# Optimization experiments

Measured on AMD Instinct MI355X. Metric: run time of the kernel, lower is better.

Reference implementation:

```python
import jax, jax.numpy as jnp
import numpy as np

N_NODES = 50000
N_EDGES = 800000
IN_DIM = 256
OUT_DIM = 128
NUM_CLASSES = 3


def setup_inputs() -> dict:
    key = jax.random.key(0)
    ks = jax.random.split(key, 8)
    x = jax.random.normal(ks[0], (N_NODES, IN_DIM), dtype=jnp.float32)
    edge_index = jax.random.randint(ks[1], (2, N_EDGES), 0, N_NODES, dtype=jnp.int64)
    # Linear W (no bias): torch stores [out,in]; we keep [in,out] and right-multiply.
    W = jax.random.normal(ks[2], (IN_DIM, OUT_DIM), dtype=jnp.float32) * (1.0 / np.sqrt(IN_DIM))
    a = jax.random.normal(ks[3], (2 * OUT_DIM, 1), dtype=jnp.float32) * 0.05  # xavier-ish
    HID = OUT_DIM // 2
    W1 = jax.random.normal(ks[4], (OUT_DIM, HID), dtype=jnp.float32) * (1.0 / np.sqrt(OUT_DIM))
    b1 = jnp.zeros((HID,), dtype=jnp.float32)
    W2 = jax.random.normal(ks[5], (HID, NUM_CLASSES), dtype=jnp.float32) * (1.0 / np.sqrt(HID))
    b2 = jnp.zeros((NUM_CLASSES,), dtype=jnp.float32)
    return {"x": x, "edge_index": edge_index, "W": W, "a": a,
            "W1": W1, "b1": b1, "W2": W2, "b2": b2}


def reference(x, edge_index, W, a, W1, b1, W2, b2):
    # Dropout layers are identity in eval mode.
    num_nodes = x.shape[0]
    Wh = x @ W                                   # [N, out_dim]
    src, tgt = edge_index[0], edge_index[1]      # [E], [E]
    d = Wh.shape[1]
    # concat([Wh_src, Wh_tgt]) @ a == Wh_src @ a[:d] + Wh_tgt @ a[d:]
    s_src = Wh @ a[:d, 0]                        # [N]
    s_tgt = Wh @ a[d:, 0]                        # [N]
    scores = jax.nn.leaky_relu(s_src[src] + s_tgt[tgt], negative_slope=0.2)  # [E]
    # NOTE: original applies softmax over ALL edges (dim=0), not per-target segment.
    alpha = jax.nn.softmax(scores)               # [E]
    msgs = alpha[:, None] * Wh[src]              # [E, out_dim]
    x_new = jax.ops.segment_sum(msgs, tgt, num_segments=num_nodes)  # [N, out_dim]
    h = jax.nn.relu(x_new @ W1 + b1)
    evidence = jax.nn.softplus(h @ W2 + b2) + 1.0
    return (x_new, evidence)
```

## Files before the change

### kernel.cpp

```cpp
#include <hip/hip_runtime.h>
#include <hip/hip_bf16.h>
#include <math.h>

#define NN 50000
#define NE 800000
#define IND 256
#define OUTD 128
#define HIDD 64
#define NBLK 196
#define BCAP 6144

typedef __attribute__((ext_vector_type(8))) short short8;
typedef __attribute__((ext_vector_type(4))) float f32x4;
typedef __attribute__((ext_vector_type(2))) float f32x2;

static __device__ __forceinline__ unsigned short f2bf_hw(float f) {
  __hip_bfloat16 h = __float2bfloat16(f);
  return __hip_bfloat16_raw(h).x;
}
static __device__ __forceinline__ float bf2f(unsigned b) {
  return __uint_as_float(b << 16);
}

__global__ __launch_bounds__(256) void k_wconv(const float* __restrict__ W,
                                               const float* __restrict__ W1,
                                               unsigned short* __restrict__ Wt,
                                               unsigned short* __restrict__ W1t,
                                               int* __restrict__ bcursor) {
  if (blockIdx.x == 0 && threadIdx.x < NBLK)
    bcursor[threadIdx.x] = threadIdx.x * BCAP;
  int t = blockIdx.x * 256 + threadIdx.x;
  int n = t >> 8, k = t & 255;
  Wt[t] = f2bf_hw(W[k * OUTD + n]);
  if (t < HIDD * OUTD) {
    int h = t >> 7, kk = t & 127;
    W1t[t] = f2bf_hw(W1[kk * HIDD + h]);
  }
}

__global__ __launch_bounds__(256) void k_gemm(const float* __restrict__ x,
                                              const unsigned short* __restrict__ Wt,
                                              const float* __restrict__ a,
                                              unsigned* __restrict__ Whp8,
                                              float* __restrict__ s_src,
                                              float* __restrict__ s_tgt) {
  __shared__ float smem[8448];
  short* As = (short*)smem;
  short* Bs = As + 64 * 40;
  float* Cs = smem;

  const int tid  = threadIdx.x;
  const int bm   = blockIdx.x * 64;
  const int wave = tid >> 6;
  const int lane = tid & 63;
  const int l15  = lane & 15;
  const int lg   = lane >> 4;

  f32x4 acc[4][2];
#pragma unroll
  for (int i = 0; i < 4; i++)
#pragma unroll
    for (int j = 0; j < 2; j++) acc[i][j] = (f32x4){0.f, 0.f, 0.f, 0.f};

  const int arow = tid >> 2, aq = tid & 3;
  long arow_g = bm + arow; if (arow_g >= NN) arow_g = NN - 1;
  const float* xp = &x[arow_g * IND + aq * 8];
  short* asp = &As[arow * 40 + aq * 8];
  const int bn = tid >> 1, bh = tid & 1;
  const unsigned short* wtp = &Wt[bn * 256 + bh * 16];
  short* bsp = &Bs[bn * 40 + bh * 16];

  for (int k0 = 0; k0 < IND; k0 += 32) {
    float4 v0 = *(const float4*)(xp + k0);
    float4 v1 = *(const float4*)(xp + k0 + 4);
    short8 apk;
    apk[0] = (short)f2bf_hw(v0.x); apk[1] = (short)f2bf_hw(v0.y);
    apk[2] = (short)f2bf_hw(v0.z); apk[3] = (short)f2bf_hw(v0.w);
    apk[4] = (short)f2bf_hw(v1.x); apk[5] = (short)f2bf_hw(v1.y);
    apk[6] = (short)f2bf_hw(v1.z); apk[7] = (short)f2bf_hw(v1.w);
    *(short8*)asp = apk;
    *(short8*)bsp       = *(const short8*)(wtp + k0);
    *(short8*)(bsp + 8) = *(const short8*)(wtp + k0 + 8);
    __syncthreads();

    short8 af[4], bf[2];
#pragma unroll
    for (int mi = 0; mi < 4; mi++)
      af[mi] = *(const short8*)&As[(mi * 16 + l15) * 40 + lg * 8];
#pragma unroll
    for (int ni = 0; ni < 2; ni++)
      bf[ni] = *(const short8*)&Bs[(wave * 32 + ni * 16 + l15) * 40 + lg * 8];
#pragma unroll
    for (int mi = 0; mi < 4; mi++)
#pragma unroll
      for (int ni = 0; ni < 2; ni++)
        acc[mi][ni] = __builtin_amdgcn_mfma_f32_16x16x32_bf16(
            af[mi], bf[ni], acc[mi][ni], 0, 0, 0);
    __syncthreads();
  }

#pragma unroll
  for (int mi = 0; mi < 4; mi++)
#pragma unroll
    for (int ni = 0; ni < 2; ni++)
#pragma unroll
      for (int r = 0; r < 4; r++) {
        int row = mi * 16 + lg * 4 + r;
        int col = wave * 32 + ni * 16 + l15;
        Cs[row * 132 + col] = acc[mi][ni][r];
      }
  __syncthreads();

#pragma unroll
  for (int i = 0; i < 4; i++) {
    int f = tid + i * 256;
    int nd = f >> 4, seg = f & 15;
    long gnode = bm + nd;
    if (gnode < NN) {
      float4 c0 = *(const float4*)&Cs[nd * 132 + seg * 8];
      float4 c1 = *(const float4*)&Cs[nd * 132 + seg * 8 + 4];
      int u0 = __builtin_amdgcn_cvt_pk_fp8_f32(c0.x, c0.y, 0, false);
      u0     = __builtin_amdgcn_cvt_pk_fp8_f32(c0.z, c0.w, u0, true);
      int u1 = __builtin_amdgcn_cvt_pk_fp8_f32(c1.x, c1.y, 0, false);
      u1     = __builtin_amdgcn_cvt_pk_fp8_f32(c1.z, c1.w, u1, true);
      *(uint2*)&Whp8[gnode * 32 + seg * 2] = make_uint2((unsigned)u0, (unsigned)u1);
    }
  }

  {
    const int nd = tid >> 2, p = tid & 3;
    float p1 = 0.f, p2 = 0.f;
    const float* crow = &Cs[nd * 132 + p * 32];
#pragma unroll
    for (int k = 0; k < 32; k++) {
      float c = crow[k];
      p1 = fmaf(c, a[p * 32 + k], p1);
      p2 = fmaf(c, a[128 + p * 32 + k], p2);
    }
    p1 += __shfl_xor(p1, 1); p1 += __shfl_xor(p1, 2);
    p2 += __shfl_xor(p2, 1); p2 += __shfl_xor(p2, 2);
    long gnode = bm + nd;
    if (p == 0 && gnode < NN) { s_src[gnode] = p1; s_tgt[gnode] = p2; }
  }
}

__global__ __launch_bounds__(256) void k_score(const int* __restrict__ ei,
                                               const float* __restrict__ s_src,
                                               const float* __restrict__ s_tgt,
                                               int* __restrict__ bcursor,
                                               int2* __restrict__ recs_mid,
                                               float* __restrict__ bmax,
                                               float* __restrict__ bsexp) {
  __shared__ int bh[NBLK];
  __shared__ int gbase[NBLK];
  __shared__ float red[4];
  __shared__ float bmx;
  const int tid = threadIdx.x;
  const long eb = (long)blockIdx.x * 4096;
  if (tid < NBLK) bh[tid] = 0;
  __syncthreads();

  int sv[16]; int tv[16]; float scv[16];
  float mx = -1e30f;
#pragma unroll
  for (int i = 0; i < 16; i++) {
    long e = eb + i * 256 + tid;
    float sc = -1e30f;
    if (e < NE) {
      int s = ei[e];
      int t = ei[NE + e];
      float v = s_src[s] + s_tgt[t];
      sc = v > 0.f ? v : 0.2f * v;
      sv[i] = s; tv[i] = t;
      atomicAdd(&bh[t >> 8], 1);
    } else {
      tv[i] = -1;
    }
    scv[i] = sc;
    mx = fmaxf(mx, sc);
  }
  __syncthreads();
  if (tid < NBLK) {
    int c = bh[tid];
    gbase[tid] = (c > 0) ? atomicAdd(&bcursor[tid], c) : 0;
    bh[tid] = 0;
  }
  __syncthreads();
#pragma unroll
  for (int i = 0; i < 16; i++) {
    if (tv[i] >= 0) {
      int b = tv[i] >> 8;
      int off = atomicAdd(&bh[b], 1);
      recs_mid[gbase[b] + off] = make_int2(sv[i] | ((tv[i] & 255) << 16),
                                           __float_as_int(scv[i]));
    }
  }

#pragma unroll
  for (int off = 32; off; off >>= 1) mx = fmaxf(mx, __shfl_down(mx, off));
  int w = tid >> 6, lane = tid & 63;
  if (lane == 0) red[w] = mx;
  __syncthreads();
  if (tid == 0) bmx = fmaxf(fmaxf(red[0], red[1]), fmaxf(red[2], red[3]));
  __syncthreads();
  const float M = bmx;
  float s = 0.f;
#pragma unroll
  for (int i = 0; i < 16; i++) s += __expf(scv[i] - M);
#pragma unroll
  for (int off = 32; off; off >>= 1) s += __shfl_down(s, off);
  if (lane == 0) red[w] = s;
  __syncthreads();
  if (tid == 0) {
    bmax[blockIdx.x] = M;
    bsexp[blockIdx.x] = red[0] + red[1] + red[2] + red[3];
  }
}

__global__ __launch_bounds__(256) void k_stats(const float* __restrict__ bmax,
                                               const float* __restrict__ bsexp,
                                               float* __restrict__ softstat) {
  __shared__ float fred[256];
  int tid = threadIdx.x;
  float m = (tid < NBLK) ? bmax[tid] : -1e30f;
  fred[tid] = m;
  __syncthreads();
  for (int off = 128; off; off >>= 1) {
    if (tid < off) fred[tid] = fmaxf(fred[tid], fred[tid + off]);
    __syncthreads();
  }
  const float M = fred[0];
  __syncthreads();
  float se = (tid < NBLK) ? bsexp[tid] * __expf(bmax[tid] - M) : 0.f;
  fred[tid] = se;
  __syncthreads();
  for (int off = 128; off; off >>= 1) {
    if (tid < off) fred[tid] += fred[tid + off];
    __syncthreads();
  }
  if (tid == 0) { softstat[0] = M; softstat[1] = fred[0]; }
}

__global__ __launch_bounds__(256) void k_sortB(const int* __restrict__ bcursor,
                                               const int2* __restrict__ recs_mid,
                                               const float* __restrict__ softstat,
                                               unsigned* __restrict__ recs,
                                               int* __restrict__ offs,
                                               int* __restrict__ cnt) {
  __shared__ int h[256], sc[256], cur[256];
  __shared__ unsigned srt[BCAP];
  const int tid = threadIdx.x;
  const int b = blockIdx.x;
  const int base = b * BCAP;
  const int m = bcursor[b] - base;
  const float M = softstat[0];
  const float inv = 1.0f / softstat[1];

  h[tid] = 0;
  __syncthreads();
  for (int i = tid; i < m; i += 256) {
    int2 r = recs_mid[base + i];
    atomicAdd(&h[(r.x >> 16) & 255], 1);
  }
  __syncthreads();
  sc[tid] = h[tid];
  __syncthreads();
  for (int off = 1; off < 256; off <<= 1) {
    int t = (tid >= off) ? sc[tid - off] : 0;
    __syncthreads();
    sc[tid] += t;
    __syncthreads();
  }
  int excl = sc[tid] - h[tid];
  cur[tid] = excl;
  offs[b * 256 + tid] = base + excl;
  cnt[b * 256 + tid] = h[tid];
  __syncthreads();
  for (int i = tid; i < m; i += 256) {
    int2 r = recs_mid[base + i];
    int tl = (r.x >> 16) & 255;
    int p = atomicAdd(&cur[tl], 1);
    float al = __expf(__int_as_float(r.y) - M) * inv;
    if (p < BCAP)
      srt[p] = (unsigned)(r.x & 0xffff) | ((unsigned)f2bf_hw(al) << 16);
  }
  __syncthreads();
  for (int i = tid; i < m; i += 256)
    recs[base + i] = srt[i];
}

__global__ __launch_bounds__(256) void k_gather(const int* __restrict__ offs,
                                                const int* __restrict__ cnt,
                                                const unsigned* __restrict__ recs,
                                                const unsigned short* __restrict__ Whp8,
                                                float* __restrict__ xnew) {
  int wid = (blockIdx.x * 256 + threadIdx.x) >> 6;
  int lane = threadIdx.x & 63;
  int start = offs[wid];
  int n = cnt[wid];
  float2 acc = make_float2(0.f, 0.f);
  for (int base = 0; base < n; base += 64) {
    int m = n - base; if (m > 64) m = 64;
    int li = lane < m ? lane : m - 1;
    unsigned r = recs[start + base + li];
    for (int i = 0; i < m; i += 8) {
      unsigned rv[8];
#pragma unroll
      for (int j = 0; j < 8; j++) rv[j] = __shfl(r, i + j);
      unsigned short v[8];
#pragma unroll
      for (int j = 0; j < 8; j++)
        v[j] = Whp8[(long)(rv[j] & 0xffffu) * 64 + lane];
#pragma unroll
      for (int j = 0; j < 8; j++) {
        float al = (i + j < m) ? bf2f(rv[j] >> 16) : 0.f;
        f32x2 w = __builtin_amdgcn_cvt_pk_f32_fp8((int)(unsigned)v[j], false);
        acc.x = fmaf(al, w[0], acc.x);
        acc.y = fmaf(al, w[1], acc.y);
      }
    }
  }
  ((float2*)xnew)[(long)wid * 64 + lane] = acc;
}

__global__ __launch_bounds__(256) void k_mlp(const float* __restrict__ xnew,
                                             const unsigned short* __restrict__ W1t,
                                             const float* __restrict__ b1,
                                             const float* __restrict__ W2,
                                             const float* __restrict__ b2,
                                             float* __restrict__ evid) {
  __shared__ short smem[17408];
  short* As = smem;
  short* Bs = smem + 64 * 136;
  float* Cs = (float*)smem;

  const int tid = threadIdx.x;
  const int nb = blockIdx.x * 64;
  const int wave = tid >> 6;
  const int lane = tid & 63;
  const int l15 = lane & 15, lg = lane >> 4;

  {
    int row = tid >> 2, seg = tid & 3;
    long g = nb + row; if (g >= NN) g = NN - 1;
    const float* xp = &xnew[g * OUTD + seg * 32];
    short* dst = &As[row * 136 + seg * 32];
    const unsigned short* wp = &W1t[row * 128 + seg * 32];
    short* wdst = &Bs[row * 136 + seg * 32];
#pragma unroll
    for (int q = 0; q < 4; q++) {
      float4 v0 = *(const float4*)(xp + q * 8);
      float4 v1 = *(const float4*)(xp + q * 8 + 4);
      short8 pk;
      pk[0] = (short)f2bf_hw(v0.x); pk[1] = (short)f2bf_hw(v0.y);
      pk[2] = (short)f2bf_hw(v0.z); pk[3] = (short)f2bf_hw(v0.w);
      pk[4] = (short)f2bf_hw(v1.x); pk[5] = (short)f2bf_hw(v1.y);
      pk[6] = (short)f2bf_hw(v1.z); pk[7] = (short)f2bf_hw(v1.w);
      *(short8*)(dst + q * 8) = pk;
      *(short8*)(wdst + q * 8) = *(const short8*)(wp + q * 8);
    }
  }
  __syncthreads();

  f32x4 acc[4];
#pragma unroll
  for (int mi = 0; mi < 4; mi++) acc[mi] = (f32x4){0.f, 0.f, 0.f, 0.f};
#pragma unroll
  for (int ks = 0; ks < 4; ks++) {
    short8 bfr = *(const short8*)&Bs[(wave * 16 + l15) * 136 + ks * 32 + lg * 8];
#pragma unroll
    for (int mi = 0; mi < 4; mi++) {
      short8 afr = *(const short8*)&As[(mi * 16 + l15) * 136 + ks * 32 + lg * 8];
      acc[mi] = __builtin_amdgcn_mfma_f32_16x16x32_bf16(afr, bfr, acc[mi], 0, 0, 0);
    }
  }
  __syncthreads();
#pragma unroll
  for (int mi = 0; mi < 4; mi++)
#pragma unroll
    for (int r = 0; r < 4; r++) {
      int row = mi * 16 + lg * 4 + r;
      int col = wave * 16 + l15;
      Cs[row * 68 + col] = acc[mi][r];
    }
  __syncthreads();

  const int ty = tid >> 4, tx = tid & 15;
  float b1r[4], w2r[4][3];
#pragma unroll
  for (int j = 0; j < 4; j++) {
    int jg = tx * 4 + j;
    b1r[j] = b1[jg];
    w2r[j][0] = W2[jg * 3 + 0];
    w2r[j][1] = W2[jg * 3 + 1];
    w2r[j][2] = W2[jg * 3 + 2];
  }
#pragma unroll
  for (int i = 0; i < 4; i++) {
    float p0 = 0.f, p1 = 0.f, p2 = 0.f;
#pragma unroll
    for (int j = 0; j < 4; j++) {
      float h = fmaxf(Cs[(ty * 4 + i) * 68 + tx * 4 + j] + b1r[j], 0.f);
      p0 = fmaf(h, w2r[j][0], p0);
      p1 = fmaf(h, w2r[j][1], p1);
      p2 = fmaf(h, w2r[j][2], p2);
    }
#pragma unroll
    for (int m = 1; m < 16; m <<= 1) {
      p0 += __shfl_xor(p0, m);
      p1 += __shfl_xor(p1, m);
      p2 += __shfl_xor(p2, m);
    }
    if (tx == 0) {
      int n = nb + ty * 4 + i;
      if (n < NN) {
        float e0 = p0 + b2[0], e1 = p1 + b2[1], e2 = p2 + b2[2];
        float s0 = e0 > 20.f ? e0 : log1pf(expf(e0));
        float s1 = e1 > 20.f ? e1 : log1pf(expf(e1));
        float s2 = e2 > 20.f ? e2 : log1pf(expf(e2));
        evid[(long)n * 3 + 0] = s0 + 1.0f;
        evid[(long)n * 3 + 1] = s1 + 1.0f;
        evid[(long)n * 3 + 2] = s2 + 1.0f;
      }
    }
  }
}

extern "C" void kernel_launch(void* const* d_in, const int* in_sizes, int n_in,
                              void* d_out, int out_size, void* d_ws, size_t ws_size,
                              hipStream_t stream) {
  const float* x   = (const float*)d_in[0];
  const int*   ei  = (const int*)d_in[1];
  const float* W   = (const float*)d_in[2];
  const float* a   = (const float*)d_in[3];
  const float* W1  = (const float*)d_in[4];
  const float* b1  = (const float*)d_in[5];
  const float* W2  = (const float*)d_in[6];
  const float* b2  = (const float*)d_in[7];

  float* xnew = (float*)d_out;
  float* evid = (float*)d_out + (size_t)NN * OUTD;

  float* wsf = (float*)d_ws;
  unsigned* Whp8     = (unsigned*)wsf;
  float*    s_src    = wsf + 1600000;
  float*    s_tgt    = wsf + 1650000;
  int2*     recs_mid = (int2*)(wsf + 1700000);
  unsigned* recs     = (unsigned*)(wsf + 4108448);
  int*      offs     = (int*)(wsf + 5312672);
  int*      cnt      = (int*)(wsf + 5362848);
  int*      bcursor  = (int*)(wsf + 5413024);
  float*    bmax     = wsf + 5413220;
  float*    bsexp    = wsf + 5413416;
  float*    softstat = wsf + 5413612;
  unsigned short* Wt  = (unsigned short*)(wsf + 5413616);
  unsigned short* W1t = (unsigned short*)(wsf + 5430000);

  k_wconv<<<128, 256, 0, stream>>>(W, W1, Wt, W1t, bcursor);
  k_gemm<<<(NN + 63) / 64, 256, 0, stream>>>(x, Wt, a, Whp8, s_src, s_tgt);
  k_score<<<NBLK, 256, 0, stream>>>(ei, s_src, s_tgt, bcursor, recs_mid, bmax, bsexp);
  k_stats<<<1, 256, 0, stream>>>(bmax, bsexp, softstat);
  k_sortB<<<NBLK, 256, 0, stream>>>(bcursor, recs_mid, softstat, recs, offs, cnt);
  k_gather<<<NN / 4, 256, 0, stream>>>(offs, cnt, recs, (const unsigned short*)Whp8, xnew);
  k_mlp<<<(NN + 63) / 64, 256, 0, stream>>>(xnew, W1t, b1, W2, b2, evid);
}
```

Baseline: 110.7 us.

## Fuse softmax stats into sort, widen GEMM K-tile, shrink MLP tile

Removes the single-block k_stats launch by having every k_sortB block redundantly reduce the 196 block max/sum-exp values. The projection GEMM stages a 64-wide K slice per iteration instead of 32, halving the loop trips and barrier count at the cost of more LDS. The MLP kernel processes 32 nodes per block instead of 64 to create more blocks. The redundant reduction adds a little work to each sort block.

```diff
diff --git a/kernel.cpp b/kernel.cpp
--- a/kernel.cpp
+++ b/kernel.cpp
@@ -46,7 +46,7 @@
                                               float* __restrict__ s_tgt) {
   __shared__ float smem[8448];
   short* As = (short*)smem;
-  short* Bs = As + 64 * 40;
+  short* Bs = As + 64 * 72;
   float* Cs = smem;
 
   const int tid  = threadIdx.x;
@@ -64,38 +64,52 @@
 
   const int arow = tid >> 2, aq = tid & 3;
   long arow_g = bm + arow; if (arow_g >= NN) arow_g = NN - 1;
-  const float* xp = &x[arow_g * IND + aq * 8];
-  short* asp = &As[arow * 40 + aq * 8];
+  const float* xp = &x[arow_g * IND + aq * 16];
+  short* asp = &As[arow * 72 + aq * 16];
   const int bn = tid >> 1, bh = tid & 1;
-  const unsigned short* wtp = &Wt[bn * 256 + bh * 16];
-  short* bsp = &Bs[bn * 40 + bh * 16];
-
-  for (int k0 = 0; k0 < IND; k0 += 32) {
-    float4 v0 = *(const float4*)(xp + k0);
-    float4 v1 = *(const float4*)(xp + k0 + 4);
-    short8 apk;
-    apk[0] = (short)f2bf_hw(v0.x); apk[1] = (short)f2bf_hw(v0.y);
-    apk[2] = (short)f2bf_hw(v0.z); apk[3] = (short)f2bf_hw(v0.w);
-    apk[4] = (short)f2bf_hw(v1.x); apk[5] = (short)f2bf_hw(v1.y);
-    apk[6] = (short)f2bf_hw(v1.z); apk[7] = (short)f2bf_hw(v1.w);
-    *(short8*)asp = apk;
-    *(short8*)bsp       = *(const short8*)(wtp + k0);
-    *(short8*)(bsp + 8) = *(const short8*)(wtp + k0 + 8);
-    __syncthreads();
-
-    short8 af[4], bf[2];
+  const unsigned short* wtp = &Wt[bn * 256 + bh * 32];
+  short* bsp = &Bs[bn * 72 + bh * 32];
+
+  for (int k0 = 0; k0 < IND; k0 += 64) {
+    float4 va0 = *(const float4*)(xp + k0);
+    float4 va1 = *(const float4*)(xp + k0 + 4);
+    float4 va2 = *(const float4*)(xp + k0 + 8);
+    float4 va3 = *(const float4*)(xp + k0 + 12);
+    short8 apk0, apk1;
+    apk0[0] = (short)f2bf_hw(va0.x); apk0[1] = (short)f2bf_hw(va0.y);
+    apk0[2] = (short)f2bf_hw(va0.z); apk0[3] = (short)f2bf_hw(va0.w);
+    apk0[4] = (short)f2bf_hw(va1.x); apk0[5] = (short)f2bf_hw(va1.y);
+    apk0[6] = (short)f2bf_hw(va1.z); apk0[7] = (short)f2bf_hw(va1.w);
+    apk1[0] = (short)f2bf_hw(va2.x); apk1[1] = (short)f2bf_hw(va2.y);
+    apk1[2] = (short)f2bf_hw(va2.z); apk1[3] = (short)f2bf_hw(va2.w);
+    apk1[4] = (short)f2bf_hw(va3.x); apk1[5] = (short)f2bf_hw(va3.y);
+    apk1[6] = (short)f2bf_hw(va3.z); apk1[7] = (short)f2bf_hw(va3.w);
+    *(short8*)asp       = apk0;
+    *(short8*)(asp + 8) = apk1;
+#pragma unroll
+    for (int q = 0; q < 4; q++)
+      *(short8*)(bsp + q * 8) = *(const short8*)(wtp + k0 + q * 8);
+    __syncthreads();
+
+    short8 af[4][2], bf[2][2];
 #pragma unroll
     for (int mi = 0; mi < 4; mi++)
-      af[mi] = *(const short8*)&As[(mi * 16 + l15) * 40 + lg * 8];
+#pragma unroll
+      for (int ks = 0; ks < 2; ks++)
+        af[mi][ks] = *(const short8*)&As[(mi * 16 + l15) * 72 + ks * 32 + lg * 8];
 #pragma unroll
     for (int ni = 0; ni < 2; ni++)
-      bf[ni] = *(const short8*)&Bs[(wave * 32 + ni * 16 + l15) * 40 + lg * 8];
-#pragma unroll
-    for (int mi = 0; mi < 4; mi++)
-#pragma unroll
-      for (int ni = 0; ni < 2; ni++)
-        acc[mi][ni] = __builtin_amdgcn_mfma_f32_16x16x32_bf16(
-            af[mi], bf[ni], acc[mi][ni], 0, 0, 0);
+#pragma unroll
+      for (int ks = 0; ks < 2; ks++)
+        bf[ni][ks] = *(const short8*)&Bs[(wave * 32 + ni * 16 + l15) * 72 + ks * 32 + lg * 8];
+#pragma unroll
+    for (int ks = 0; ks < 2; ks++)
+#pragma unroll
+      for (int mi = 0; mi < 4; mi++)
+#pragma unroll
+        for (int ni = 0; ni < 2; ni++)
+          acc[mi][ni] = __builtin_amdgcn_mfma_f32_16x16x32_bf16(
+              af[mi][ks], bf[ni][ks], acc[mi][ni], 0, 0, 0);
     __syncthreads();
   }
 
@@ -217,44 +231,38 @@
   }
 }
 
-__global__ __launch_bounds__(256) void k_stats(const float* __restrict__ bmax,
-                                               const float* __restrict__ bsexp,
-                                               float* __restrict__ softstat) {
-  __shared__ float fred[256];
-  int tid = threadIdx.x;
-  float m = (tid < NBLK) ? bmax[tid] : -1e30f;
-  fred[tid] = m;
-  __syncthreads();
-  for (int off = 128; off; off >>= 1) {
-    if (tid < off) fred[tid] = fmaxf(fred[tid], fred[tid + off]);
-    __syncthreads();
-  }
-  const float M = fred[0];
-  __syncthreads();
-  float se = (tid < NBLK) ? bsexp[tid] * __expf(bmax[tid] - M) : 0.f;
-  fred[tid] = se;
-  __syncthreads();
-  for (int off = 128; off; off >>= 1) {
-    if (tid < off) fred[tid] += fred[tid + off];
-    __syncthreads();
-  }
-  if (tid == 0) { softstat[0] = M; softstat[1] = fred[0]; }
-}
-
 __global__ __launch_bounds__(256) void k_sortB(const int* __restrict__ bcursor,
                                                const int2* __restrict__ recs_mid,
-                                               const float* __restrict__ softstat,
+                                               const float* __restrict__ bmax,
+                                               const float* __restrict__ bsexp,
                                                unsigned* __restrict__ recs,
                                                int* __restrict__ offs,
                                                int* __restrict__ cnt) {
+  __shared__ float fred[256];
   __shared__ int h[256], sc[256], cur[256];
   __shared__ unsigned srt[BCAP];
   const int tid = threadIdx.x;
   const int b = blockIdx.x;
   const int base = b * BCAP;
   const int m = bcursor[b] - base;
-  const float M = softstat[0];
-  const float inv = 1.0f / softstat[1];
+
+  float mv = (tid < NBLK) ? bmax[tid] : -1e30f;
+  fred[tid] = mv;
+  __syncthreads();
+  for (int off = 128; off; off >>= 1) {
+    if (tid < off) fred[tid] = fmaxf(fred[tid], fred[tid + off]);
+    __syncthreads();
+  }
+  const float M = fred[0];
+  __syncthreads();
+  float se = (tid < NBLK) ? bsexp[tid] * __expf(bmax[tid] - M) : 0.f;
+  fred[tid] = se;
+  __syncthreads();
+  for (int off = 128; off; off >>= 1) {
+    if (tid < off) fred[tid] += fred[tid + off];
+    __syncthreads();
+  }
+  const float inv = 1.0f / fred[0];
 
   h[tid] = 0;
   __syncthreads();
@@ -329,26 +337,24 @@
                                              const float* __restrict__ W2,
                                              const float* __restrict__ b2,
                                              float* __restrict__ evid) {
-  __shared__ short smem[17408];
+  __shared__ short smem[13056];
   short* As = smem;
-  short* Bs = smem + 64 * 136;
+  short* Bs = smem + 32 * 136;
   float* Cs = (float*)smem;
 
   const int tid = threadIdx.x;
-  const int nb = blockIdx.x * 64;
+  const int nb = blockIdx.x * 32;
   const int wave = tid >> 6;
   const int lane = tid & 63;
   const int l15 = lane & 15, lg = lane >> 4;
 
   {
-    int row = tid >> 2, seg = tid & 3;
+    int row = tid >> 3, seg = tid & 7;
     long g = nb + row; if (g >= NN) g = NN - 1;
-    const float* xp = &xnew[g * OUTD + seg * 32];
-    short* dst = &As[row * 136 + seg * 32];
-    const unsigned short* wp = &W1t[row * 128 + seg * 32];
-    short* wdst = &Bs[row * 136 + seg * 32];
-#pragma unroll
-    for (int q = 0; q < 4; q++) {
+    const float* xp = &xnew[g * OUTD + seg * 16];
+    short* dst = &As[row * 136 + seg * 16];
+#pragma unroll
+    for (int q = 0; q < 2; q++) {
       float4 v0 = *(const float4*)(xp + q * 8);
       float4 v1 = *(const float4*)(xp + q * 8 + 4);
       short8 pk;
@@ -357,26 +363,31 @@
       pk[4] = (short)f2bf_hw(v1.x); pk[5] = (short)f2bf_hw(v1.y);
       pk[6] = (short)f2bf_hw(v1.z); pk[7] = (short)f2bf_hw(v1.w);
       *(short8*)(dst + q * 8) = pk;
+    }
+    int wrow = tid >> 2, wseg = tid & 3;
+    const unsigned short* wp = &W1t[wrow * 128 + wseg * 32];
+    short* wdst = &Bs[wrow * 136 + wseg * 32];
+#pragma unroll
+    for (int q = 0; q < 4; q++)
       *(short8*)(wdst + q * 8) = *(const short8*)(wp + q * 8);
-    }
-  }
-  __syncthreads();
-
-  f32x4 acc[4];
-#pragma unroll
-  for (int mi = 0; mi < 4; mi++) acc[mi] = (f32x4){0.f, 0.f, 0.f, 0.f};
+  }
+  __syncthreads();
+
+  f32x4 acc[2];
+#pragma unroll
+  for (int mi = 0; mi < 2; mi++) acc[mi] = (f32x4){0.f, 0.f, 0.f, 0.f};
 #pragma unroll
   for (int ks = 0; ks < 4; ks++) {
     short8 bfr = *(const short8*)&Bs[(wave * 16 + l15) * 136 + ks * 32 + lg * 8];
 #pragma unroll
-    for (int mi = 0; mi < 4; mi++) {
+    for (int mi = 0; mi < 2; mi++) {
       short8 afr = *(const short8*)&As[(mi * 16 + l15) * 136 + ks * 32 + lg * 8];
       acc[mi] = __builtin_amdgcn_mfma_f32_16x16x32_bf16(afr, bfr, acc[mi], 0, 0, 0);
     }
   }
   __syncthreads();
 #pragma unroll
-  for (int mi = 0; mi < 4; mi++)
+  for (int mi = 0; mi < 2; mi++)
 #pragma unroll
     for (int r = 0; r < 4; r++) {
       int row = mi * 16 + lg * 4 + r;
@@ -396,11 +407,11 @@
     w2r[j][2] = W2[jg * 3 + 2];
   }
 #pragma unroll
-  for (int i = 0; i < 4; i++) {
+  for (int i = 0; i < 2; i++) {
     float p0 = 0.f, p1 = 0.f, p2 = 0.f;
 #pragma unroll
     for (int j = 0; j < 4; j++) {
-      float h = fmaxf(Cs[(ty * 4 + i) * 68 + tx * 4 + j] + b1r[j], 0.f);
+      float h = fmaxf(Cs[(ty * 2 + i) * 68 + tx * 4 + j] + b1r[j], 0.f);
       p0 = fmaf(h, w2r[j][0], p0);
       p1 = fmaf(h, w2r[j][1], p1);
       p2 = fmaf(h, w2r[j][2], p2);
@@ -412,7 +423,7 @@
       p2 += __shfl_xor(p2, m);
     }
     if (tx == 0) {
-      int n = nb + ty * 4 + i;
+      int n = nb + ty * 2 + i;
       if (n < NN) {
         float e0 = p0 + b2[0], e1 = p1 + b2[1], e2 = p2 + b2[2];
         float s0 = e0 > 20.f ? e0 : log1pf(expf(e0));
@@ -452,15 +463,13 @@
   int*      bcursor  = (int*)(wsf + 5413024);
   float*    bmax     = wsf + 5413220;
   float*    bsexp    = wsf + 5413416;
-  float*    softstat = wsf + 5413612;
   unsigned short* Wt  = (unsigned short*)(wsf + 5413616);
   unsigned short* W1t = (unsigned short*)(wsf + 5430000);
 
   k_wconv<<<128, 256, 0, stream>>>(W, W1, Wt, W1t, bcursor);
   k_gemm<<<(NN + 63) / 64, 256, 0, stream>>>(x, Wt, a, Whp8, s_src, s_tgt);
   k_score<<<NBLK, 256, 0, stream>>>(ei, s_src, s_tgt, bcursor, recs_mid, bmax, bsexp);
-  k_stats<<<1, 256, 0, stream>>>(bmax, bsexp, softstat);
-  k_sortB<<<NBLK, 256, 0, stream>>>(bcursor, recs_mid, softstat, recs, offs, cnt);
+  k_sortB<<<NBLK, 256, 0, stream>>>(bcursor, recs_mid, bmax, bsexp, recs, offs, cnt);
   k_gather<<<NN / 4, 256, 0, stream>>>(offs, cnt, recs, (const unsigned short*)Whp8, xnew);
-  k_mlp<<<(NN + 63) / 64, 256, 0, stream>>>(xnew, W1t, b1, W2, b2, evid);
-}
+  k_mlp<<<(NN + 31) / 32, 256, 0, stream>>>(xnew, W1t, b1, W2, b2, evid);
+}
```

Result: faster. 103.6 us (-6.4%).
